# Optimization experiments

Measured on AMD Instinct MI355X. Metric: run time of the kernel, lower is better.

The kernel has to match this reference:

```python
import jax, jax.numpy as jnp
import numpy as np

B, T, D = 2, 2048, 2048
H = 16
HD = D // H  # 128


def _rotate_half(x):
    x1, x2 = x[..., :HD // 2], x[..., HD // 2:]
    return jnp.concatenate((-x2, x1), axis=-1)


def setup_inputs() -> dict:
    key = jax.random.key(0)
    ks = jax.random.split(key, 7)
    return {
        "x": jax.random.normal(ks[0], (B, T, D), dtype=jnp.float32),
        "rope_cos": jax.random.uniform(ks[1], (1, 1, T, HD), dtype=jnp.float32),
        "rope_sin": jax.random.uniform(ks[2], (1, 1, T, HD), dtype=jnp.float32),
        "qkv_w": jax.random.normal(ks[3], (3 * D, D), dtype=jnp.float32) * (1.0 / np.sqrt(D)),
        "qkv_b": jax.random.normal(ks[4], (3 * D,), dtype=jnp.float32) * 0.02,
        "out_w": jax.random.normal(ks[5], (D, D), dtype=jnp.float32) * (1.0 / np.sqrt(D)),
        "out_b": jax.random.normal(ks[6], (D,), dtype=jnp.float32) * 0.02,
    }


def reference(x, rope_cos, rope_sin, qkv_w, qkv_b, out_w, out_b):
    bsz, t, d = x.shape
    # fused QKV projection (torch Linear: x @ W.T + b)
    qkv = x @ qkv_w.T + qkv_b                       # [B, T, 3D]
    qkv = qkv.reshape(bsz, t, 3, H, HD).transpose(2, 0, 3, 1, 4)  # [3, B, H, T, HD]
    q, k, v = qkv[0], qkv[1], qkv[2]
    # RoPE
    cos = rope_cos[:, :, :t, :]
    sin = rope_sin[:, :, :t, :]
    q = q * cos + _rotate_half(q) * sin
    k = k * cos + _rotate_half(k) * sin
    # causal SDPA (eval mode -> no dropout)
    scale = 1.0 / np.sqrt(HD)
    scores = jnp.einsum("bhqd,bhkd->bhqk", q, k) * scale
    causal = jnp.tril(jnp.ones((t, t), dtype=bool))
    scores = jnp.where(causal, scores, jnp.finfo(scores.dtype).min)
    attn = jax.nn.softmax(scores, axis=-1)
    out = jnp.einsum("bhqk,bhkd->bhqd", attn, v)    # [B, H, T, HD]
    out = out.transpose(0, 2, 1, 3).reshape(bsz, t, d)
    return out @ out_w.T + out_b
```

## Files before the change

kernel.cpp:

```cpp
#include <hip/hip_runtime.h>

typedef unsigned short u16;
typedef __attribute__((ext_vector_type(8))) short bf16x8;
typedef __attribute__((ext_vector_type(4))) float f32x4;

__device__ __forceinline__ float bf2f(unsigned int u) {
    union { unsigned int i; float f; } x; x.i = u << 16; return x.f;
}
__device__ __forceinline__ u16 f2bf(float f) {
    union { float f; unsigned int i; } x; x.f = f;
    unsigned int r = x.i + 0x7fffu + ((x.i >> 16) & 1u);
    return (u16)(r >> 16);
}

__device__ __forceinline__ void gl2lds16(const u16* g, u16* l) {
    __builtin_amdgcn_global_load_lds(
        (const __attribute__((address_space(1))) unsigned int*)g,
        (__attribute__((address_space(3))) unsigned int*)l, 16, 0, 0);
}

#define NX  8388608
#define NW1 12582912
#define NW2 4194304
__global__ __launch_bounds__(256) void convert_kernel(
    const float* __restrict__ x, const float* __restrict__ w1,
    const float* __restrict__ w2, u16* __restrict__ dst)
{
    const int i = (blockIdx.x * 256 + threadIdx.x) * 4;
    const float* src;
    int off;
    if (i < NX)            { src = x;  off = i; }
    else if (i < NX + NW1) { src = w1; off = i - NX; }
    else                   { src = w2; off = i - NX - NW1; }
    float4 v = *(const float4*)(src + off);
    ushort4 o;
    o.x = f2bf(v.x); o.y = f2bf(v.y); o.z = f2bf(v.z); o.w = f2bf(v.w);
    *(ushort4*)(dst + i) = o;
}

#define NTILES 64
#define BUFSZ  12288

#define GEMM_SETUP(Ag, Bg)                                                    \
    const int tid = threadIdx.x;                                              \
    const int wave = tid >> 6, lane = tid & 63;                               \
    const int l16 = lane & 15, quad = lane >> 4;                              \
    const int wr = wave >> 2, wc = wave & 3;                                  \
    f32x4 acc[4][4];                                                          \
    _Pragma("unroll") for (int mi = 0; mi < 4; ++mi)                          \
        _Pragma("unroll") for (int ni = 0; ni < 4; ++ni)                      \
            acc[mi][ni] = (f32x4){0.f, 0.f, 0.f, 0.f};                        \
    int aoff[4], boff[4];                                                     \
    _Pragma("unroll") for (int mi = 0; mi < 4; ++mi) {                        \
        const int r = wr * 64 + mi * 16 + l16;                                \
        aoff[mi] = r * 32 + ((quad ^ ((r >> 1) & 3)) << 3);                   \
    }                                                                         \
    _Pragma("unroll") for (int ni = 0; ni < 4; ++ni) {                        \
        const int r = (wc >> 1) * 128 + (ni >> 1) * 64 + (wc & 1) * 32        \
                    + (ni & 1) * 16 + l16;                                    \
        boff[ni] = 4096 + r * 32 + ((quad ^ ((r >> 1) & 3)) << 3);            \
    }                                                                         \
    const u16* sbase[3]; int sdst[3];                                         \
    _Pragma("unroll") for (int j = 0; j < 3; ++j) {                           \
        const int c = wave * 3 + j;                                           \
        const int g = lane & 3;                                               \
        int r; const u16* bp; int d;                                          \
        if (c < 8) {                                                          \
            r = c * 16 + (lane >> 2);                                         \
            bp = Ag + (size_t)(m0 + r) * 2048;                                \
            d = c * 512 + lane * 8;                                           \
        } else {                                                              \
            r = (c - 8) * 16 + (lane >> 2);                                   \
            bp = Bg + (size_t)(n0 + r) * 2048;                                \
            d = 4096 + (c - 8) * 512 + lane * 8;                              \
        }                                                                     \
        sbase[j] = bp + ((g ^ ((r >> 1) & 3)) << 3);                          \
        sdst[j] = d;                                                          \
    }                                                                         \
       \
    _Pragma("unroll") for (int pt = 0; pt < 3; ++pt)                          \
        _Pragma("unroll") for (int j = 0; j < 3; ++j)                         \
            gl2lds16(sbase[j] + pt * 32, lds + pt * BUFSZ + sdst[j]);         \
    bf16x8 afr[2][4], bfr[2][4];                                              \
    asm volatile("s_waitcnt vmcnt(6)" ::: "memory");                          \
    __builtin_amdgcn_s_barrier();                                             \
    _Pragma("unroll") for (int mi = 0; mi < 4; ++mi)                          \
        afr[0][mi] = *(const bf16x8*)(lds + aoff[mi]);                        \
    _Pragma("unroll") for (int ni = 0; ni < 4; ++ni)                          \
        bfr[0][ni] = *(const bf16x8*)(lds + boff[ni]);

#define GPH(TT, SLOT, PAR, STG, VMN, RD, LGN)                                 \
    {                                                                         \
        if (STG) {                                                            \
            u16* nb = lds + (((SLOT) + 3) & 3) * BUFSZ;                       \
            _Pragma("unroll") for (int j = 0; j < 3; ++j)                     \
                gl2lds16(sbase[j] + ((TT) + 3) * 32, nb + sdst[j]);           \
        }                                                                     \
        asm volatile("s_waitcnt vmcnt(" #VMN ")" ::: "memory");               \
        __builtin_amdgcn_s_barrier();                                         \
        if (RD) {                                                             \
            const u16* rb = lds + (((SLOT) + 1) & 3) * BUFSZ;                 \
            _Pragma("unroll") for (int mi = 0; mi < 4; ++mi)                  \
                afr[(PAR) ^ 1][mi] = *(const bf16x8*)(rb + aoff[mi]);         \
            _Pragma("unroll") for (int ni = 0; ni < 4; ++ni)                  \
                bfr[(PAR) ^ 1][ni] = *(const bf16x8*)(rb + boff[ni]);         \
        }                                                                     \
        asm volatile("s_waitcnt lgkmcnt(" #LGN ")" ::: "memory");             \
        __builtin_amdgcn_sched_barrier(0);                                    \
        __builtin_amdgcn_s_setprio(1);                                        \
        _Pragma("unroll") for (int mi = 0; mi < 4; ++mi)                      \
            _Pragma("unroll") for (int ni = 0; ni < 4; ++ni)                  \
                acc[mi][ni] = __builtin_amdgcn_mfma_f32_16x16x32_bf16(        \
                    afr[PAR][mi], bfr[PAR][ni], acc[mi][ni], 0, 0, 0);        \
        __builtin_amdgcn_s_setprio(0);                                        \
        __builtin_amdgcn_sched_barrier(0);                                    \
        __builtin_amdgcn_s_barrier();                                         \
    }

#define GEMM_MAIN()                                                           \
    for (int t = 0; t < 15; ++t) {                                            \
        const int T = t * 4;                                                  \
        GPH(T,     0, 0, 1, 6, 1, 8)                                          \
        GPH(T + 1, 1, 1, 1, 6, 1, 8)                                          \
        GPH(T + 2, 2, 0, 1, 6, 1, 8)                                          \
        GPH(T + 3, 3, 1, 1, 6, 1, 8)                                          \
    }                                                                         \
    GPH(60, 0, 0, 1, 6, 1, 8)                                                 \
    GPH(61, 1, 1, 0, 3, 1, 8)                                                 \
    GPH(62, 2, 0, 0, 0, 1, 8)                                                 \
    GPH(63, 3, 1, 0, 0, 0, 0)

__global__ __launch_bounds__(512, 2) void qkv8_kernel(
    const u16* __restrict__ xb, const u16* __restrict__ wb,
    const float* __restrict__ bias, const float* __restrict__ rc,
    const float* __restrict__ rs, u16* __restrict__ Qo,
    u16* __restrict__ Ko, u16* __restrict__ Vo)
{
    __shared__ u16 lds[4 * BUFSZ];
    const int bid = blockIdx.x;
    const int swz = (bid & 7) * 96 + (bid >> 3);
    const int m0 = (swz & 31) * 128;
    const int n0 = (swz >> 5) * 256;

    GEMM_SETUP(xb, wb)
    GEMM_MAIN()

    const int e  = n0 >> 11;
    const int h  = ((n0 & 2047) >> 7) + (wc >> 1);
    const int hb = n0 + (wc >> 1) * 128;
    const int hq = wc & 1;
    if (e < 2) {
        u16* dst = (e == 0) ? Qo : Ko;
        #pragma unroll
        for (int mi = 0; mi < 4; ++mi) {
            #pragma unroll
            for (int r = 0; r < 4; ++r) {
                const int m = m0 + wr * 64 + mi * 16 + quad * 4 + r;
                const int b = m >> 11, tt = m & 2047;
                u16* drow = dst + ((size_t)(b * 16 + h) * 2048 + tt) * 128;
                const float* crow = rc + tt * 128;
                const float* sr2  = rs + tt * 128;
                #pragma unroll
                for (int p = 0; p < 2; ++p) {
                    const int hd1 = hq * 32 + p * 16 + l16;
                    const int hd2 = hd1 + 64;
                    const float v1 = acc[mi][p][r]     + bias[hb + hd1];
                    const float v2 = acc[mi][p + 2][r] + bias[hb + hd2];
                    drow[hd1] = f2bf(v1 * crow[hd1] - v2 * sr2[hd1]);
                    drow[hd2] = f2bf(v2 * crow[hd2] + v1 * sr2[hd2]);
                }
            }
        }
    } else {
        #pragma unroll
        for (int mi = 0; mi < 4; ++mi) {
            const int mb = m0 + wr * 64 + mi * 16 + quad * 4;
            const int b = mb >> 11, tt = mb & 2047;
            u16* vbase = Vo + (size_t)(b * 16 + h) * 128 * 2048 + tt;
            #pragma unroll
            for (int ni = 0; ni < 4; ++ni) {
                const int hd = (ni >> 1) * 64 + hq * 32 + (ni & 1) * 16 + l16;
                const float bs = bias[hb + hd];
                ushort4 o;
                #pragma unroll
                for (int r = 0; r < 4; ++r)
                    ((u16*)&o)[r] = f2bf(acc[mi][ni][r] + bs);
                *(ushort4*)(vbase + (size_t)hd * 2048) = o;
            }
        }
    }
}

#define KPAD 136
#define VPAD 72
#define PPAD 72

__global__ __launch_bounds__(256) void attn_mfma_kernel(
    const u16* __restrict__ Qi, const u16* __restrict__ Ki,
    const u16* __restrict__ Vg, u16* __restrict__ Oo)
{
    __shared__ u16 Ks[64 * KPAD];
    __shared__ u16 Vt[128 * VPAD];
    __shared__ u16 Ps[4][16 * PPAD];

    const int tid  = threadIdx.x;
    const int wave = tid >> 6, lane = tid & 63;
    const int l16 = lane & 15, quad = lane >> 4;
    const int bh = blockIdx.y;
    const size_t base = (size_t)bh * (2048 * 128);

    const int qtile[2] = { (int)blockIdx.x, 31 - (int)blockIdx.x };

    bf16x8 qf[2][4];
    f32x4 o[2][8];
    float l_i[2][4];
    #pragma unroll
    for (int s = 0; s < 2; ++s) {
        const u16* qp = Qi + base + (size_t)(qtile[s] * 64 + wave * 16 + l16) * 128 + quad * 8;
        #pragma unroll
        for (int c = 0; c < 4; ++c) qf[s][c] = *(const bf16x8*)(qp + c * 32);
        #pragma unroll
        for (int i = 0; i < 8; ++i) o[s][i] = (f32x4){0.f, 0.f, 0.f, 0.f};
        #pragma unroll
        for (int r = 0; r < 4; ++r) l_i[s][r] = 0.f;
    }

    const float scale = 0.08838834764831845f;
    const int ntiles = qtile[1] + 1;

    for (int t = 0; t < ntiles; ++t) {
        const int kt = t * 64;
        __syncthreads();
        {
            const int key = tid >> 2, d0 = (tid & 3) * 32;
            const u16* src = Ki + base + (size_t)(kt + key) * 128 + d0;
            u16* dst = Ks + key * KPAD + d0;
            #pragma unroll
            for (int i = 0; i < 4; ++i)
                *(bf16x8*)(dst + 8 * i) = *(const bf16x8*)(src + 8 * i);
        }
        {
            const int d = tid >> 1, koff = (tid & 1) * 32;
            const u16* src = Vg + ((size_t)bh * 128 + d) * 2048 + kt + koff;
            u16* dst = Vt + d * VPAD + koff;
            #pragma unroll
            for (int i = 0; i < 4; ++i)
                *(bf16x8*)(dst + 8 * i) = *(const bf16x8*)(src + 8 * i);
        }
        __syncthreads();

        const bool act_a = (t <= qtile[0]);

        f32x4 sa[4], sb[4];
        #pragma unroll
        for (int nt = 0; nt < 4; ++nt) {
            sa[nt] = (f32x4){0.f, 0.f, 0.f, 0.f};
            sb[nt] = (f32x4){0.f, 0.f, 0.f, 0.f};
            #pragma unroll
            for (int c = 0; c < 4; ++c) {
                bf16x8 kf = *(const bf16x8*)(Ks + (nt * 16 + l16) * KPAD + c * 32 + quad * 8);
                sb[nt] = __builtin_amdgcn_mfma_f32_16x16x32_bf16(qf[1][c], kf, sb[nt], 0, 0, 0);
                sa[nt] = __builtin_amdgcn_mfma_f32_16x16x32_bf16(qf[0][c], kf, sa[nt], 0, 0, 0);
            }
        }

        #pragma unroll
        for (int s = 0; s < 2; ++s) {
            if (s == 0 && !act_a) continue;
            f32x4* sc = (s == 0) ? sa : sb;
            const int qrow = qtile[s] * 64 + wave * 16 + quad * 4;
            const bool diag = (t == qtile[s]);

            #pragma unroll
            for (int nt = 0; nt < 4; ++nt) {
                #pragma unroll
                for (int r = 0; r < 4; ++r) {
                    float v = sc[nt][r] * scale - 11.0f;
                    if (diag) {
                        const int key = kt + nt * 16 + l16;
                        v = (key <= qrow + r) ? v : -1.0e30f;
                    }
                    const float e = __expf(v);
                    sc[nt][r] = e;
                    l_i[s][r] += e;
                }
            }

            u16* pw = Ps[wave];
            #pragma unroll
            for (int nt = 0; nt < 4; ++nt)
                #pragma unroll
                for (int r = 0; r < 4; ++r)
                    pw[(quad * 4 + r) * PPAD + nt * 16 + l16] = f2bf(sc[nt][r]);

            bf16x8 pf0 = *(const bf16x8*)(pw + l16 * PPAD + quad * 8);
            bf16x8 pf1 = *(const bf16x8*)(pw + l16 * PPAD + 32 + quad * 8);

            #pragma unroll
            for (int nt = 0; nt < 8; ++nt) {
                bf16x8 vf0 = *(const bf16x8*)(Vt + (nt * 16 + l16) * VPAD + quad * 8);
                bf16x8 vf1 = *(const bf16x8*)(Vt + (nt * 16 + l16) * VPAD + 32 + quad * 8);
                o[s][nt] = __builtin_amdgcn_mfma_f32_16x16x32_bf16(pf0, vf0, o[s][nt], 0, 0, 0);
                o[s][nt] = __builtin_amdgcn_mfma_f32_16x16x32_bf16(pf1, vf1, o[s][nt], 0, 0, 0);
            }
        }
    }

    const int b = bh >> 4, h = bh & 15;
    #pragma unroll
    for (int s = 0; s < 2; ++s) {
        const int qrow = qtile[s] * 64 + wave * 16 + quad * 4;
        #pragma unroll
        for (int r = 0; r < 4; ++r) {
            float ls = l_i[s][r];
            ls += __shfl_xor(ls, 1, 16);
            ls += __shfl_xor(ls, 2, 16);
            ls += __shfl_xor(ls, 4, 16);
            ls += __shfl_xor(ls, 8, 16);
            const float inv = 1.f / ls;
            u16* orow = Oo + ((size_t)(b * 2048 + qrow + r)) * 2048 + h * 128 + l16;
            #pragma unroll
            for (int nt = 0; nt < 8; ++nt)
                orow[nt * 16] = f2bf(o[s][nt][r] * inv);
        }
    }
}

__global__ __launch_bounds__(512, 2) void proj8_kernel(
    const u16* __restrict__ A, const u16* __restrict__ wb,
    const float* __restrict__ bias, float* __restrict__ out)
{
    __shared__ u16 lds[4 * BUFSZ];
    const int bid = blockIdx.x;
    const int swz = (bid & 7) * 32 + (bid >> 3);
    const int m0 = (swz & 31) * 128;
    const int n0 = (swz >> 5) * 256;

    GEMM_SETUP(A, wb)
    GEMM_MAIN()

    #pragma unroll
    for (int mi = 0; mi < 4; ++mi) {
        #pragma unroll
        for (int r = 0; r < 4; ++r) {
            const int m = m0 + wr * 64 + mi * 16 + quad * 4 + r;
            float* orow = out + (size_t)m * 2048;
            #pragma unroll
            for (int ni = 0; ni < 4; ++ni) {
                const int n = n0 + (wc >> 1) * 128 + (ni >> 1) * 64
                            + (wc & 1) * 32 + (ni & 1) * 16 + l16;
                orow[n] = acc[mi][ni][r] + bias[n];
            }
        }
    }
}

extern "C" void kernel_launch(void* const* d_in, const int* in_sizes, int n_in,
                              void* d_out, int out_size, void* d_ws, size_t ws_size,
                              hipStream_t stream) {
    const float* x     = (const float*)d_in[0];
    const float* rcos  = (const float*)d_in[1];
    const float* rsin  = (const float*)d_in[2];
    const float* qkv_w = (const float*)d_in[3];
    const float* qkv_b = (const float*)d_in[4];
    const float* out_w = (const float*)d_in[5];
    const float* out_b = (const float*)d_in[6];
    float* out = (float*)d_out;

    const size_t NE = (size_t)2 * 16 * 2048 * 128;
    u16* Q      = (u16*)d_ws;
    u16* K      = Q + NE;
    u16* V      = K + NE;
    u16* xb     = V + NE;
    u16* O      = xb;
    u16* qkv_wb = xb + NX;
    u16* out_wb = qkv_wb + NW1;

    convert_kernel<<<dim3((NX + NW1 + NW2) / 1024), 256, 0, stream>>>(
        x, qkv_w, out_w, xb);
    qkv8_kernel<<<dim3(768), 512, 0, stream>>>(
        xb, qkv_wb, qkv_b, rcos, rsin, Q, K, V);
    attn_mfma_kernel<<<dim3(16, 32), 256, 0, stream>>>(Q, K, V, O);
    proj8_kernel<<<dim3(256), 512, 0, stream>>>(O, out_wb, out_b, out);
}
```

Measured before the change: 380.4 us.

## Enlarge GEMM block tile to 256x256 and drop register double-buffering

```diff
diff --git a/kernel.cpp b/kernel.cpp
--- a/kernel.cpp
+++ b/kernel.cpp
@@ -39,96 +39,90 @@
 }
 
 #define NTILES 64
-#define BUFSZ  12288
+#define BUFSZ  16384
 
 #define GEMM_SETUP(Ag, Bg)                                                    \
     const int tid = threadIdx.x;                                              \
     const int wave = tid >> 6, lane = tid & 63;                               \
     const int l16 = lane & 15, quad = lane >> 4;                              \
     const int wr = wave >> 2, wc = wave & 3;                                  \
-    f32x4 acc[4][4];                                                          \
-    _Pragma("unroll") for (int mi = 0; mi < 4; ++mi)                          \
+    f32x4 acc[8][4];                                                          \
+    _Pragma("unroll") for (int mi = 0; mi < 8; ++mi)                          \
         _Pragma("unroll") for (int ni = 0; ni < 4; ++ni)                      \
             acc[mi][ni] = (f32x4){0.f, 0.f, 0.f, 0.f};                        \
-    int aoff[4], boff[4];                                                     \
-    _Pragma("unroll") for (int mi = 0; mi < 4; ++mi) {                        \
-        const int r = wr * 64 + mi * 16 + l16;                                \
+    int aoff[8], boff[4];                                                     \
+    _Pragma("unroll") for (int mi = 0; mi < 8; ++mi) {                        \
+        const int r = wr * 128 + mi * 16 + l16;                               \
         aoff[mi] = r * 32 + ((quad ^ ((r >> 1) & 3)) << 3);                   \
     }                                                                         \
     _Pragma("unroll") for (int ni = 0; ni < 4; ++ni) {                        \
         const int r = (wc >> 1) * 128 + (ni >> 1) * 64 + (wc & 1) * 32        \
                     + (ni & 1) * 16 + l16;                                    \
-        boff[ni] = 4096 + r * 32 + ((quad ^ ((r >> 1) & 3)) << 3);            \
+        boff[ni] = 8192 + r * 32 + ((quad ^ ((r >> 1) & 3)) << 3);            \
     }                                                                         \
-    const u16* sbase[3]; int sdst[3];                                         \
-    _Pragma("unroll") for (int j = 0; j < 3; ++j) {                           \
-        const int c = wave * 3 + j;                                           \
+    const u16* sbase[4]; int sdst[4];                                         \
+    _Pragma("unroll") for (int j = 0; j < 4; ++j) {                           \
+        const int c = wave * 4 + j;                                           \
         const int g = lane & 3;                                               \
         int r; const u16* bp; int d;                                          \
-        if (c < 8) {                                                          \
+        if (c < 16) {                                                         \
             r = c * 16 + (lane >> 2);                                         \
             bp = Ag + (size_t)(m0 + r) * 2048;                                \
             d = c * 512 + lane * 8;                                           \
         } else {                                                              \
-            r = (c - 8) * 16 + (lane >> 2);                                   \
+            r = (c - 16) * 16 + (lane >> 2);                                  \
             bp = Bg + (size_t)(n0 + r) * 2048;                                \
-            d = 4096 + (c - 8) * 512 + lane * 8;                              \
+            d = 8192 + (c - 16) * 512 + lane * 8;                             \
         }                                                                     \
         sbase[j] = bp + ((g ^ ((r >> 1) & 3)) << 3);                          \
         sdst[j] = d;                                                          \
     }                                                                         \
        \
     _Pragma("unroll") for (int pt = 0; pt < 3; ++pt)                          \
-        _Pragma("unroll") for (int j = 0; j < 3; ++j)                         \
-            gl2lds16(sbase[j] + pt * 32, lds + pt * BUFSZ + sdst[j]);         \
-    bf16x8 afr[2][4], bfr[2][4];                                              \
-    asm volatile("s_waitcnt vmcnt(6)" ::: "memory");                          \
-    __builtin_amdgcn_s_barrier();                                             \
-    _Pragma("unroll") for (int mi = 0; mi < 4; ++mi)                          \
-        afr[0][mi] = *(const bf16x8*)(lds + aoff[mi]);                        \
-    _Pragma("unroll") for (int ni = 0; ni < 4; ++ni)                          \
-        bfr[0][ni] = *(const bf16x8*)(lds + boff[ni]);
-
-#define GPH(TT, SLOT, PAR, STG, VMN, RD, LGN)                                 \
+        _Pragma("unroll") for (int j = 0; j < 4; ++j)                         \
+            gl2lds16(sbase[j] + pt * 32, lds + pt * BUFSZ + sdst[j]);
+
+#define GPH(TT, RSL, SSL, STG, VMN)                                           \
     {                                                                         \
         if (STG) {                                                            \
-            u16* nb = lds + (((SLOT) + 3) & 3) * BUFSZ;                       \
-            _Pragma("unroll") for (int j = 0; j < 3; ++j)                     \
+            u16* nb = lds + (SSL) * BUFSZ;                                    \
+            _Pragma("unroll") for (int j = 0; j < 4; ++j)                     \
                 gl2lds16(sbase[j] + ((TT) + 3) * 32, nb + sdst[j]);           \
         }                                                                     \
         asm volatile("s_waitcnt vmcnt(" #VMN ")" ::: "memory");               \
         __builtin_amdgcn_s_barrier();                                         \
-        if (RD) {                                                             \
-            const u16* rb = lds + (((SLOT) + 1) & 3) * BUFSZ;                 \
-            _Pragma("unroll") for (int mi = 0; mi < 4; ++mi)                  \
-                afr[(PAR) ^ 1][mi] = *(const bf16x8*)(rb + aoff[mi]);         \
+        {                                                                     \
+            const u16* rb = lds + (RSL) * BUFSZ;                              \
+            bf16x8 af[8], bf[4];                                              \
+            _Pragma("unroll") for (int mi = 0; mi < 8; ++mi)                  \
+                af[mi] = *(const bf16x8*)(rb + aoff[mi]);                     \
             _Pragma("unroll") for (int ni = 0; ni < 4; ++ni)                  \
-                bfr[(PAR) ^ 1][ni] = *(const bf16x8*)(rb + boff[ni]);         \
+                bf[ni] = *(const bf16x8*)(rb + boff[ni]);                     \
+            asm volatile("s_waitcnt lgkmcnt(0)" ::: "memory");                \
+            __builtin_amdgcn_sched_barrier(0);                                \
+            __builtin_amdgcn_s_setprio(1);                                    \
+            _Pragma("unroll") for (int mi = 0; mi < 8; ++mi)                  \
+                _Pragma("unroll") for (int ni = 0; ni < 4; ++ni)              \
+                    acc[mi][ni] = __builtin_amdgcn_mfma_f32_16x16x32_bf16(    \
+                        af[mi], bf[ni], acc[mi][ni], 0, 0, 0);                \
+            __builtin_amdgcn_s_setprio(0);                                    \
+            __builtin_amdgcn_sched_barrier(0);                                \
+            __builtin_amdgcn_s_barrier();                                     \
         }                                                                     \
-        asm volatile("s_waitcnt lgkmcnt(" #LGN ")" ::: "memory");             \
-        __builtin_amdgcn_sched_barrier(0);                                    \
-        __builtin_amdgcn_s_setprio(1);                                        \
-        _Pragma("unroll") for (int mi = 0; mi < 4; ++mi)                      \
-            _Pragma("unroll") for (int ni = 0; ni < 4; ++ni)                  \
-                acc[mi][ni] = __builtin_amdgcn_mfma_f32_16x16x32_bf16(        \
-                    afr[PAR][mi], bfr[PAR][ni], acc[mi][ni], 0, 0, 0);        \
-        __builtin_amdgcn_s_setprio(0);                                        \
-        __builtin_amdgcn_sched_barrier(0);                                    \
-        __builtin_amdgcn_s_barrier();                                         \
     }
 
 #define GEMM_MAIN()                                                           \
     for (int t = 0; t < 15; ++t) {                                            \
         const int T = t * 4;                                                  \
-        GPH(T,     0, 0, 1, 6, 1, 8)                                          \
-        GPH(T + 1, 1, 1, 1, 6, 1, 8)                                          \
-        GPH(T + 2, 2, 0, 1, 6, 1, 8)                                          \
-        GPH(T + 3, 3, 1, 1, 6, 1, 8)                                          \
+        GPH(T,     0, 3, 1, 8)                                                \
+        GPH(T + 1, 1, 0, 1, 8)                                                \
+        GPH(T + 2, 2, 1, 1, 8)                                                \
+        GPH(T + 3, 3, 2, 1, 8)                                                \
     }                                                                         \
-    GPH(60, 0, 0, 1, 6, 1, 8)                                                 \
-    GPH(61, 1, 1, 0, 3, 1, 8)                                                 \
-    GPH(62, 2, 0, 0, 0, 1, 8)                                                 \
-    GPH(63, 3, 1, 0, 0, 0, 0)
+    GPH(60, 0, 3, 1, 8)                                                       \
+    GPH(61, 1, 0, 0, 8)                                                       \
+    GPH(62, 2, 1, 0, 4)                                                       \
+    GPH(63, 3, 2, 0, 0)
 
 __global__ __launch_bounds__(512, 2) void qkv8_kernel(
     const u16* __restrict__ xb, const u16* __restrict__ wb,
@@ -138,9 +132,9 @@
 {
     __shared__ u16 lds[4 * BUFSZ];
     const int bid = blockIdx.x;
-    const int swz = (bid & 7) * 96 + (bid >> 3);
-    const int m0 = (swz & 31) * 128;
-    const int n0 = (swz >> 5) * 256;
+    const int xcd = bid & 7, j = bid >> 3;
+    const int m0 = (xcd * 2 + (j & 1)) * 256;
+    const int n0 = (j >> 1) * 256;
 
     GEMM_SETUP(xb, wb)
     GEMM_MAIN()
@@ -152,10 +146,10 @@
     if (e < 2) {
         u16* dst = (e == 0) ? Qo : Ko;
         #pragma unroll
-        for (int mi = 0; mi < 4; ++mi) {
+        for (int mi = 0; mi < 8; ++mi) {
             #pragma unroll
             for (int r = 0; r < 4; ++r) {
-                const int m = m0 + wr * 64 + mi * 16 + quad * 4 + r;
+                const int m = m0 + wr * 128 + mi * 16 + quad * 4 + r;
                 const int b = m >> 11, tt = m & 2047;
                 u16* drow = dst + ((size_t)(b * 16 + h) * 2048 + tt) * 128;
                 const float* crow = rc + tt * 128;
@@ -173,8 +167,8 @@
         }
     } else {
         #pragma unroll
-        for (int mi = 0; mi < 4; ++mi) {
-            const int mb = m0 + wr * 64 + mi * 16 + quad * 4;
+        for (int mi = 0; mi < 8; ++mi) {
+            const int mb = m0 + wr * 128 + mi * 16 + quad * 4;
             const int b = mb >> 11, tt = mb & 2047;
             u16* vbase = Vo + (size_t)(b * 16 + h) * 128 * 2048 + tt;
             #pragma unroll
@@ -332,18 +326,18 @@
 {
     __shared__ u16 lds[4 * BUFSZ];
     const int bid = blockIdx.x;
-    const int swz = (bid & 7) * 32 + (bid >> 3);
-    const int m0 = (swz & 31) * 128;
-    const int n0 = (swz >> 5) * 256;
+    const int xcd = bid & 7, j = bid >> 3;
+    const int m0 = (xcd * 2 + (j & 1)) * 256;
+    const int n0 = (j >> 1) * 256;
 
     GEMM_SETUP(A, wb)
     GEMM_MAIN()
 
     #pragma unroll
-    for (int mi = 0; mi < 4; ++mi) {
+    for (int mi = 0; mi < 8; ++mi) {
         #pragma unroll
         for (int r = 0; r < 4; ++r) {
-            const int m = m0 + wr * 64 + mi * 16 + quad * 4 + r;
+            const int m = m0 + wr * 128 + mi * 16 + quad * 4 + r;
             float* orow = out + (size_t)m * 2048;
             #pragma unroll
             for (int ni = 0; ni < 4; ++ni) {
@@ -378,8 +372,8 @@
 
     convert_kernel<<<dim3((NX + NW1 + NW2) / 1024), 256, 0, stream>>>(
         x, qkv_w, out_w, xb);
-    qkv8_kernel<<<dim3(768), 512, 0, stream>>>(
+    qkv8_kernel<<<dim3(384), 512, 0, stream>>>(
         xb, qkv_wb, qkv_b, rcos, rsin, Q, K, V);
     attn_mfma_kernel<<<dim3(16, 32), 256, 0, stream>>>(Q, K, V, O);
-    proj8_kernel<<<dim3(256), 512, 0, stream>>>(O, out_wb, out_b, out);
-}
+    proj8_kernel<<<dim3(128), 512, 0, stream>>>(O, out_wb, out_b, out);
+}
```

Measured after the change: 415.7 us. +9.3%, slower.
